# Optimization experiments

Hardware: AMD Instinct MI355X
Metric: run time of the kernel (lower is better)

## Reference

```python
import jax, jax.numpy as jnp
import numpy as np

N_NODES = 50000
N_EDGES = 800000
HID = 256
OUT = 128
NEG_SLOPE = 0.2


def gat_layer(x, src, dst, W_src, W_dst, a_src_vec, a_dst_vec, bias, n_nodes):
    # Dense projections (PyG lin_src / lin_dst for tuple in_channels)
    h_src = x @ W_src              # [N, C]
    h_dst = x @ W_dst              # [N, C]
    # Per-node attention logits (att_src/att_dst dot products)
    a_src = h_src @ a_src_vec      # [N]
    a_dst = h_dst @ a_dst_vec      # [N]
    # Edge logits + LeakyReLU
    e = jax.nn.leaky_relu(a_src[src] + a_dst[dst], NEG_SLOPE)  # [E]
    # Segment softmax over incoming edges of each dst node
    m = jax.ops.segment_max(e, dst, num_segments=n_nodes)      # [N]
    m = jnp.where(jnp.isfinite(m), m, 0.0)                      # empty segments
    ex = jnp.exp(e - m[dst])                                    # [E]
    s = jax.ops.segment_sum(ex, dst, num_segments=n_nodes)     # [N]
    alpha = ex / (s[dst] + 1e-16)                               # [E]
    # Attention-weighted message aggregation (scatter-add to dst)
    msg = alpha[:, None] * h_src[src]                           # [E, C]
    out = jax.ops.segment_sum(msg, dst, num_segments=n_nodes)  # [N, C]
    return out + bias


def setup_inputs() -> dict:
    key = jax.random.key(0)
    ks = jax.random.split(key, 12)
    x = jax.random.normal(ks[0], (N_NODES, HID), dtype=jnp.float32)
    edge_index = jax.random.randint(ks[1], (2, N_EDGES), 0, N_NODES, dtype=jnp.int64)
    sc1 = 1.0 / np.sqrt(HID)
    sc2 = 1.0 / np.sqrt(HID)
    return {
        "x": x,
        "edge_index": edge_index,
        "W1_src": jax.random.normal(ks[2], (HID, HID), dtype=jnp.float32) * sc1,
        "W1_dst": jax.random.normal(ks[3], (HID, HID), dtype=jnp.float32) * sc1,
        "att1_src": jax.random.normal(ks[4], (HID,), dtype=jnp.float32) * sc1,
        "att1_dst": jax.random.normal(ks[5], (HID,), dtype=jnp.float32) * sc1,
        "b1": jnp.zeros((HID,), dtype=jnp.float32),
        "W2_src": jax.random.normal(ks[6], (HID, OUT), dtype=jnp.float32) * sc2,
        "W2_dst": jax.random.normal(ks[7], (HID, OUT), dtype=jnp.float32) * sc2,
        "att2_src": jax.random.normal(ks[8], (OUT,), dtype=jnp.float32) * (1.0 / np.sqrt(OUT)),
        "att2_dst": jax.random.normal(ks[9], (OUT,), dtype=jnp.float32) * (1.0 / np.sqrt(OUT)),
        "b2": jnp.zeros((OUT,), dtype=jnp.float32),
    }


def reference(x, edge_index, W1_src, W1_dst, att1_src, att1_dst, b1,
              W2_src, W2_dst, att2_src, att2_dst, b2):
    src, dst = edge_index[0], edge_index[1]
    h = gat_layer(x, src, dst, W1_src, W1_dst, att1_src, att1_dst, b1, N_NODES)
    h = jax.nn.relu(h)
    out = gat_layer(h, src, dst, W2_src, W2_dst, att2_src, att2_dst, b2, N_NODES)
    return out
```

## Files before the change

### kernel.cpp

```cpp
#include <hip/hip_runtime.h>
#include <math.h>

#define N_NODES 50000
#define N_EDGES 800000
#define HID 256
#define OUT_C 128
#define NEG_SLOPE 0.2f
#define SCAN_NB ((N_NODES + 255) / 256)

typedef __attribute__((ext_vector_type(8))) short bf16x8;
typedef __attribute__((ext_vector_type(4))) float f32x4;
typedef _Float16 half_t;
typedef __attribute__((ext_vector_type(4))) _Float16 half4;
typedef __attribute__((ext_vector_type(2))) _Float16 half2t;

__device__ inline unsigned short bf16_rne(float x) {
    unsigned u = __float_as_uint(x);
    return (unsigned short)((u + 0x7fffu + ((u >> 16) & 1u)) >> 16);
}

__device__ __forceinline__ void async_copy16(const void* g, void* l) {
    __builtin_amdgcn_global_load_lds(
        (const __attribute__((address_space(1))) unsigned int*)g,
        (__attribute__((address_space(3))) unsigned int*)l, 16, 0, 0);
}


__global__ __launch_bounds__(256) void hist_rank_kernel(
    const int* __restrict__ dst, int* __restrict__ counts, int* __restrict__ rank) {
    int e = blockIdx.x * 256 + threadIdx.x;
    if (e < N_EDGES) rank[e] = atomicAdd(&counts[dst[e]], 1);
}

__global__ __launch_bounds__(256) void block_scan_kernel(
    const int* __restrict__ counts, int* __restrict__ excl,
    int* __restrict__ blockSums, int n) {
    __shared__ int waveSums[4];
    int i = blockIdx.x * 256 + threadIdx.x;
    int lane = threadIdx.x & 63;
    int wv = threadIdx.x >> 6;
    int c = (i < n) ? counts[i] : 0;
    int v = c;
    #pragma unroll
    for (int off = 1; off < 64; off <<= 1) {
        int t = __shfl_up(v, off);
        if (lane >= off) v += t;
    }
    if (lane == 63) waveSums[wv] = v;
    __syncthreads();
    int waveOff = 0;
    #pragma unroll
    for (int w = 0; w < 4; w++)
        if (w < wv) waveOff += waveSums[w];
    if (i < n) excl[i] = waveOff + v - c;
    if (threadIdx.x == 255) blockSums[blockIdx.x] = waveOff + v;
}

__global__ __launch_bounds__(256) void add_offsets_kernel(
    int* __restrict__ excl, const int* __restrict__ blockSums, int n) {
    __shared__ int lds[4];
    int tid = threadIdx.x;
    int partial = 0;
    for (int j = tid; j < (int)blockIdx.x; j += 256) partial += blockSums[j];
    #pragma unroll
    for (int off = 32; off > 0; off >>= 1) partial += __shfl_down(partial, off);
    if ((tid & 63) == 0) lds[tid >> 6] = partial;
    __syncthreads();
    int prefix = lds[0] + lds[1] + lds[2] + lds[3];
    int i = blockIdx.x * 256 + tid;
    if (i < n) excl[i] += prefix;
    if (i == 0) excl[n] = N_EDGES;
}

__global__ __launch_bounds__(256) void scatter_kernel(
    const int* __restrict__ src, const int* __restrict__ dst,
    const int* __restrict__ offsets, const int* __restrict__ rank,
    int* __restrict__ src_sorted) {
    int e = blockIdx.x * 256 + threadIdx.x;
    if (e >= N_EDGES) return;
    src_sorted[offsets[dst[e]] + rank[e]] = src[e];
}


__global__ __launch_bounds__(64) void compute_v_all_kernel(
    const float* __restrict__ W1s, const float* __restrict__ att1s,
    const float* __restrict__ W1d, const float* __restrict__ att1d,
    const float* __restrict__ W2s, const float* __restrict__ att2s,
    const float* __restrict__ W2d, const float* __restrict__ att2d,
    float* __restrict__ v1s, float* __restrict__ v1d,
    float* __restrict__ v2s, float* __restrict__ v2d) {
    int k = blockIdx.x;
    int lane = threadIdx.x;
    const float* W; const float* att; float* v; int cout;
    switch (blockIdx.y) {
        case 0: W = W1s; att = att1s; v = v1s; cout = HID; break;
        case 1: W = W1d; att = att1d; v = v1d; cout = HID; break;
        case 2: W = W2s; att = att2s; v = v2s; cout = OUT_C; break;
        default: W = W2d; att = att2d; v = v2d; cout = OUT_C; break;
    }
    float sum = 0.f;
    for (int j = lane; j < cout; j += 64)
        sum += W[k * cout + j] * att[j];
    #pragma unroll
    for (int off = 32; off > 0; off >>= 1)
        sum += __shfl_down(sum, off);
    if (lane == 0) v[k] = sum;
}


#define PACK1_T (8 * 17 * 64)
#define PACK2_T (8 * 9 * 64)

__global__ __launch_bounds__(256) void pack_all_kernel(
    const float* __restrict__ W1, const float* __restrict__ v1s, const float* __restrict__ v1d,
    const float* __restrict__ W2, const float* __restrict__ v2s, const float* __restrict__ v2d,
    unsigned short* __restrict__ hi1, unsigned short* __restrict__ lo1,
    unsigned short* __restrict__ hi2, unsigned short* __restrict__ lo2) {
    int t = blockIdx.x * 256 + threadIdx.x;
    const float *W, *vs, *vd; unsigned short *hi, *lo; int cout, NTL, tt;
    if (t < PACK1_T)            { tt = t;           W = W1; vs = v1s; vd = v1d; hi = hi1; lo = lo1; cout = HID;  NTL = 17; }
    else if (t < PACK1_T + PACK2_T) { tt = t - PACK1_T; W = W2; vs = v2s; vd = v2d; hi = hi2; lo = lo2; cout = OUT_C; NTL = 9; }
    else return;
    int lane = tt & 63;
    int tile = (tt >> 6) % NTL;
    int ks = tt / (64 * NTL);
    int m = lane & 15;
    int kbase = ks * 32 + (lane >> 4) * 8;
    #pragma unroll
    for (int j = 0; j < 8; j++) {
        float val;
        if (tile < NTL - 1) val = W[(kbase + j) * cout + tile * 16 + m];
        else val = (m == 0) ? vs[kbase + j] : (m == 1) ? vd[kbase + j] : 0.f;
        unsigned short h = bf16_rne(val);
        hi[tt * 8 + j] = h;
        lo[tt * 8 + j] = bf16_rne(val - __uint_as_float((unsigned)h << 16));
    }
}


template <int COUT, int NT, bool WRITE_A>
__device__ __forceinline__ void gemm_body(
    const float* __restrict__ A, const unsigned short* __restrict__ Bhi,
    const unsigned short* __restrict__ Blo, half_t* __restrict__ H,
    float* __restrict__ a_s, float* __restrict__ a_d, int M, int tile0,
    short* sBh, short* sBl) {
    const int NTL = COUT / 16 + 1;
    int wave = threadIdx.x >> 6, lane = threadIdx.x & 63;
    int m = lane & 15, quad = lane >> 4;
    int row0 = blockIdx.x * 128 + wave * 32;
    f32x4 acc[2][NT];
    #pragma unroll
    for (int rg = 0; rg < 2; rg++)
        #pragma unroll
        for (int nt = 0; nt < NT; nt++)
            acc[rg][nt] = (f32x4){0.f, 0.f, 0.f, 0.f};

    const float* arow[2];
    #pragma unroll
    for (int rg = 0; rg < 2; rg++) {
        int r = row0 + rg * 16 + m;
        if (r >= M) r = M - 1;
        arow[rg] = A + (size_t)r * HID;
    }

    for (int ks = 0; ks < 8; ks++) {
        __syncthreads();
        for (int u = wave; u < 2 * NT; u += 4) {
            int nt = (u < NT) ? u : u - NT;
            int tile = (WRITE_A && nt == NT - 1) ? (COUT / 16) : (tile0 + nt);
            size_t goff = ((size_t)(ks * NTL + tile) * 64 + lane) * 8;
            if (u < NT) async_copy16(Bhi + goff, sBh + nt * 512);
            else        async_copy16(Blo + goff, sBl + nt * 512);
        }
        __syncthreads();

        bf16x8 ah[2], al[2];
        #pragma unroll
        for (int rg = 0; rg < 2; rg++) {
            const float* ap = arow[rg] + ks * 32 + quad * 8;
            float4 v0 = *(const float4*)ap;
            float4 v1 = *(const float4*)(ap + 4);
            float av[8] = {v0.x, v0.y, v0.z, v0.w, v1.x, v1.y, v1.z, v1.w};
            #pragma unroll
            for (int j = 0; j < 8; j++) {
                unsigned short h = bf16_rne(av[j]);
                float hf = __uint_as_float((unsigned)h << 16);
                ah[rg][j] = (short)h;
                al[rg][j] = (short)bf16_rne(av[j] - hf);
            }
        }
        #pragma unroll
        for (int nt = 0; nt < NT; nt++) {
            bf16x8 bh = *(const bf16x8*)(sBh + nt * 512 + lane * 8);
            bf16x8 bl = *(const bf16x8*)(sBl + nt * 512 + lane * 8);
            acc[0][nt] = __builtin_amdgcn_mfma_f32_16x16x32_bf16(ah[0], bh, acc[0][nt], 0, 0, 0);
            acc[1][nt] = __builtin_amdgcn_mfma_f32_16x16x32_bf16(ah[1], bh, acc[1][nt], 0, 0, 0);
            acc[0][nt] = __builtin_amdgcn_mfma_f32_16x16x32_bf16(ah[0], bl, acc[0][nt], 0, 0, 0);
            acc[1][nt] = __builtin_amdgcn_mfma_f32_16x16x32_bf16(ah[1], bl, acc[1][nt], 0, 0, 0);
            acc[0][nt] = __builtin_amdgcn_mfma_f32_16x16x32_bf16(al[0], bh, acc[0][nt], 0, 0, 0);
            acc[1][nt] = __builtin_amdgcn_mfma_f32_16x16x32_bf16(al[1], bh, acc[1][nt], 0, 0, 0);
        }
    }
    const int NW = WRITE_A ? NT - 1 : NT;
    #pragma unroll
    for (int rg = 0; rg < 2; rg++)
        #pragma unroll
        for (int nt = 0; nt < NW; nt++)
            #pragma unroll
            for (int r = 0; r < 4; r++) {
                int row = row0 + rg * 16 + quad * 4 + r;
                if (row < M)
                    H[(size_t)row * COUT + (tile0 + nt) * 16 + m] = (half_t)acc[rg][nt][r];
            }
    if (WRITE_A) {
        #pragma unroll
        for (int rg = 0; rg < 2; rg++)
            #pragma unroll
            for (int r = 0; r < 4; r++) {
                int row = row0 + rg * 16 + quad * 4 + r;
                if (row < M) {
                    if (m == 0) a_s[row] = acc[rg][NT - 1][r];
                    else if (m == 1) a_d[row] = acc[rg][NT - 1][r];
                }
            }
    }
}

template <int COUT>
__global__ __launch_bounds__(256) void mfma_gemm_a_kernel(
    const float* __restrict__ A, const unsigned short* __restrict__ Bhi,
    const unsigned short* __restrict__ Blo, half_t* __restrict__ H,
    float* __restrict__ a_s, float* __restrict__ a_d, int M) {
    __shared__ short sBh[9 * 512];
    __shared__ short sBl[9 * 512];
    if (blockIdx.y == 0)
        gemm_body<COUT, 9, true>(A, Bhi, Blo, H, a_s, a_d, M, 0, sBh, sBl);
    else
        gemm_body<COUT, 8, false>(A, Bhi, Blo, H, a_s, a_d, M, 8, sBh, sBl);
}


template <int C, bool RELU>
__global__ __launch_bounds__(256) void fused_aggregate_kernel(
    const int* __restrict__ offsets, const int* __restrict__ src_sorted,
    const float* __restrict__ a_src, const float* __restrict__ a_dst,
    const half_t* __restrict__ h, const float* __restrict__ bias,
    float* __restrict__ out) {
    constexpr int CH = 8;
    int node = (int)((blockIdx.x * 256u + threadIdx.x) >> 6);
    int lane = threadIdx.x & 63;
    if (node >= N_NODES) return;
    int beg = offsets[node], end = offsets[node + 1];
    float ad = a_dst[node];
    float s = 0.f;

    if (C == 256) {
        float4 acc = make_float4(0.f, 0.f, 0.f, 0.f);
        for (int base = beg; base < end; base += CH) {
            int cnt = end - base; if (cnt > CH) cnt = CH;
            int idx[CH];
            #pragma unroll
            for (int j = 0; j < CH; j++)
                idx[j] = src_sorted[(j < cnt) ? base + j : base];
            half4 hv[CH];
            #pragma unroll
            for (int j = 0; j < CH; j++)
                hv[j] = *(const half4*)(h + ((unsigned)idx[j] * C + lane * 4));
            float w[CH];
            #pragma unroll
            for (int j = 0; j < CH; j++) {
                float l = a_src[idx[j]] + ad;
                l = fmaxf(l, l * NEG_SLOPE);
                w[j] = (j < cnt) ? __expf(l) : 0.f;
                s += w[j];
            }
            #pragma unroll
            for (int j = 0; j < CH; j++) {
                acc.x += w[j] * (float)hv[j][0]; acc.y += w[j] * (float)hv[j][1];
                acc.z += w[j] * (float)hv[j][2]; acc.w += w[j] * (float)hv[j][3];
            }
        }
        float inv = 1.f / (s + 1e-16f);
        float4 bv = *(const float4*)(bias + lane * 4);
        acc.x = acc.x * inv + bv.x; acc.y = acc.y * inv + bv.y;
        acc.z = acc.z * inv + bv.z; acc.w = acc.w * inv + bv.w;
        if (RELU) {
            acc.x = fmaxf(acc.x, 0.f); acc.y = fmaxf(acc.y, 0.f);
            acc.z = fmaxf(acc.z, 0.f); acc.w = fmaxf(acc.w, 0.f);
        }
        *(float4*)(out + (size_t)node * C + lane * 4) = acc;
    } else {
        float2 acc = make_float2(0.f, 0.f);
        for (int base = beg; base < end; base += CH) {
            int cnt = end - base; if (cnt > CH) cnt = CH;
            int idx[CH];
            #pragma unroll
            for (int j = 0; j < CH; j++)
                idx[j] = src_sorted[(j < cnt) ? base + j : base];
            half2t hv[CH];
            #pragma unroll
            for (int j = 0; j < CH; j++)
                hv[j] = *(const half2t*)(h + ((unsigned)idx[j] * C + lane * 2));
            float w[CH];
            #pragma unroll
            for (int j = 0; j < CH; j++) {
                float l = a_src[idx[j]] + ad;
                l = fmaxf(l, l * NEG_SLOPE);
                w[j] = (j < cnt) ? __expf(l) : 0.f;
                s += w[j];
            }
            #pragma unroll
            for (int j = 0; j < CH; j++) {
                acc.x += w[j] * (float)hv[j][0]; acc.y += w[j] * (float)hv[j][1];
            }
        }
        float inv = 1.f / (s + 1e-16f);
        float2 bv = *(const float2*)(bias + lane * 2);
        acc.x = acc.x * inv + bv.x; acc.y = acc.y * inv + bv.y;
        if (RELU) { acc.x = fmaxf(acc.x, 0.f); acc.y = fmaxf(acc.y, 0.f); }
        *(float2*)(out + (size_t)node * C + lane * 2) = acc;
    }
}

extern "C" void kernel_launch(void* const* d_in, const int* in_sizes, int n_in,
                              void* d_out, int out_size, void* d_ws, size_t ws_size,
                              hipStream_t stream) {
    const float* x     = (const float*)d_in[0];
    const int*   edge  = (const int*)d_in[1];
    const int*   src   = edge;
    const int*   dst   = edge + N_EDGES;
    const float* W1s   = (const float*)d_in[2];
    const float* W1d   = (const float*)d_in[3];
    const float* att1s = (const float*)d_in[4];
    const float* att1d = (const float*)d_in[5];
    const float* b1    = (const float*)d_in[6];
    const float* W2s   = (const float*)d_in[7];
    const float* W2d   = (const float*)d_in[8];
    const float* att2s = (const float*)d_in[9];
    const float* att2d = (const float*)d_in[10];
    const float* b2    = (const float*)d_in[11];
    float* out = (float*)d_out;

    float* ws    = (float*)d_ws;
    half_t* h1   = (half_t*)ws;
    float* act2  = ws + (size_t)N_NODES * HID;
    float* a_s   = act2 + (size_t)N_NODES * HID;
    float* a_d   = a_s + N_NODES;
    float* vbuf  = a_d + N_NODES;
    int* ibase      = (int*)(vbuf + 4 * HID);
    int* src_sorted = ibase;
    int* rank       = src_sorted + N_EDGES;
    int* counts     = rank + N_EDGES;
    int* offsets    = counts + N_NODES;
    int* blockSums  = offsets + N_NODES + 1;
    unsigned short* wp1h = (unsigned short*)(((uintptr_t)(blockSums + SCAN_NB) + 15) & ~(uintptr_t)15);
    unsigned short* wp1l = wp1h + PACK1_T * 8;
    unsigned short* wp2h = wp1l + PACK1_T * 8;
    unsigned short* wp2l = wp2h + PACK2_T * 8;
    float* v1s = vbuf, *v1d = vbuf + HID, *v2s = vbuf + 2 * HID, *v2d = vbuf + 3 * HID;
    half_t* h2 = h1;

    const int edgeBlocks = (N_EDGES + 255) / 256;
    const int waveBlocksN = (N_NODES + 3) / 4;
    const int gemmBlocks = (N_NODES + 127) / 128;

    hipMemsetAsync(counts, 0, N_NODES * sizeof(int), stream);
    hist_rank_kernel<<<edgeBlocks, 256, 0, stream>>>(dst, counts, rank);
    block_scan_kernel<<<SCAN_NB, 256, 0, stream>>>(counts, offsets, blockSums, N_NODES);
    add_offsets_kernel<<<SCAN_NB, 256, 0, stream>>>(offsets, blockSums, N_NODES);
    scatter_kernel<<<edgeBlocks, 256, 0, stream>>>(src, dst, offsets, rank, src_sorted);

    compute_v_all_kernel<<<dim3(HID, 4), 64, 0, stream>>>(
        W1s, att1s, W1d, att1d, W2s, att2s, W2d, att2d, v1s, v1d, v2s, v2d);
    pack_all_kernel<<<(PACK1_T + PACK2_T + 255) / 256, 256, 0, stream>>>(
        W1s, v1s, v1d, W2s, v2s, v2d, wp1h, wp1l, wp2h, wp2l);

    mfma_gemm_a_kernel<HID><<<dim3(gemmBlocks, 2), 256, 0, stream>>>(
        x, wp1h, wp1l, h1, a_s, a_d, N_NODES);
    fused_aggregate_kernel<HID, true><<<waveBlocksN, 256, 0, stream>>>(
        offsets, src_sorted, a_s, a_d, h1, b1, act2);

    mfma_gemm_a_kernel<OUT_C><<<dim3(gemmBlocks, 1), 256, 0, stream>>>(
        act2, wp2h, wp2l, h2, a_s, a_d, N_NODES);
    fused_aggregate_kernel<OUT_C, false><<<waveBlocksN, 256, 0, stream>>>(
        offsets, src_sorted, a_s, a_d, h2, b2, out);
}
```

Baseline: 323.7 us.

## Fuse prep kernels, compute all GEMM tiles per block, double-buffer B tiles

Merges the edge scatter, attention-vector projection and weight packing into one prep kernel, folding the W·att dot products directly into packing. The layer GEMM now computes every output tile in a single block instead of splitting columns across grid.y, so each block loads and splits its A rows only once. B tiles are double-buffered in LDS so the next k-step's async copy overlaps the current MFMAs. This raises per-block accumulator registers and LDS use, and halves the block count for the first layer, which may reduce occupancy.

```diff
diff --git a/kernel.cpp b/kernel.cpp
--- a/kernel.cpp
+++ b/kernel.cpp
@@ -72,55 +72,37 @@
     if (i == 0) excl[n] = N_EDGES;
 }
 
-__global__ __launch_bounds__(256) void scatter_kernel(
+
+#define PACK1_T (8 * 17 * 64)
+#define PACK2_T (8 * 9 * 64)
+#define EDGE_BLOCKS ((N_EDGES + 255) / 256)
+#define PACK_BLOCKS ((PACK1_T + PACK2_T + 255) / 256)
+
+__global__ __launch_bounds__(256) void prep_kernel(
     const int* __restrict__ src, const int* __restrict__ dst,
     const int* __restrict__ offsets, const int* __restrict__ rank,
-    int* __restrict__ src_sorted) {
-    int e = blockIdx.x * 256 + threadIdx.x;
-    if (e >= N_EDGES) return;
-    src_sorted[offsets[dst[e]] + rank[e]] = src[e];
-}
-
-
-__global__ __launch_bounds__(64) void compute_v_all_kernel(
+    int* __restrict__ src_sorted,
     const float* __restrict__ W1s, const float* __restrict__ att1s,
     const float* __restrict__ W1d, const float* __restrict__ att1d,
     const float* __restrict__ W2s, const float* __restrict__ att2s,
     const float* __restrict__ W2d, const float* __restrict__ att2d,
-    float* __restrict__ v1s, float* __restrict__ v1d,
-    float* __restrict__ v2s, float* __restrict__ v2d) {
-    int k = blockIdx.x;
-    int lane = threadIdx.x;
-    const float* W; const float* att; float* v; int cout;
-    switch (blockIdx.y) {
-        case 0: W = W1s; att = att1s; v = v1s; cout = HID; break;
-        case 1: W = W1d; att = att1d; v = v1d; cout = HID; break;
-        case 2: W = W2s; att = att2s; v = v2s; cout = OUT_C; break;
-        default: W = W2d; att = att2d; v = v2d; cout = OUT_C; break;
-    }
-    float sum = 0.f;
-    for (int j = lane; j < cout; j += 64)
-        sum += W[k * cout + j] * att[j];
-    #pragma unroll
-    for (int off = 32; off > 0; off >>= 1)
-        sum += __shfl_down(sum, off);
-    if (lane == 0) v[k] = sum;
-}
-
-
-#define PACK1_T (8 * 17 * 64)
-#define PACK2_T (8 * 9 * 64)
-
-__global__ __launch_bounds__(256) void pack_all_kernel(
-    const float* __restrict__ W1, const float* __restrict__ v1s, const float* __restrict__ v1d,
-    const float* __restrict__ W2, const float* __restrict__ v2s, const float* __restrict__ v2d,
     unsigned short* __restrict__ hi1, unsigned short* __restrict__ lo1,
     unsigned short* __restrict__ hi2, unsigned short* __restrict__ lo2) {
-    int t = blockIdx.x * 256 + threadIdx.x;
-    const float *W, *vs, *vd; unsigned short *hi, *lo; int cout, NTL, tt;
-    if (t < PACK1_T)            { tt = t;           W = W1; vs = v1s; vd = v1d; hi = hi1; lo = lo1; cout = HID;  NTL = 17; }
-    else if (t < PACK1_T + PACK2_T) { tt = t - PACK1_T; W = W2; vs = v2s; vd = v2d; hi = hi2; lo = lo2; cout = OUT_C; NTL = 9; }
-    else return;
+    if (blockIdx.x < EDGE_BLOCKS) {
+        int e = blockIdx.x * 256 + threadIdx.x;
+        if (e < N_EDGES)
+            src_sorted[offsets[dst[e]] + rank[e]] = src[e];
+        return;
+    }
+    int t = (blockIdx.x - EDGE_BLOCKS) * 256 + threadIdx.x;
+    const float *W, *Ws, *Wd, *avs, *avd; unsigned short *hi, *lo; int cout, NTL, tt;
+    if (t < PACK1_T) {
+        tt = t; W = W1s; Ws = W1s; Wd = W1d; avs = att1s; avd = att1d;
+        hi = hi1; lo = lo1; cout = HID; NTL = 17;
+    } else if (t < PACK1_T + PACK2_T) {
+        tt = t - PACK1_T; W = W2s; Ws = W2s; Wd = W2d; avs = att2s; avd = att2d;
+        hi = hi2; lo = lo2; cout = OUT_C; NTL = 9;
+    } else return;
     int lane = tt & 63;
     int tile = (tt >> 6) % NTL;
     int ks = tt / (64 * NTL);
@@ -129,8 +111,19 @@
     #pragma unroll
     for (int j = 0; j < 8; j++) {
         float val;
-        if (tile < NTL - 1) val = W[(kbase + j) * cout + tile * 16 + m];
-        else val = (m == 0) ? vs[kbase + j] : (m == 1) ? vd[kbase + j] : 0.f;
+        if (tile < NTL - 1) {
+            val = W[(size_t)(kbase + j) * cout + tile * 16 + m];
+        } else if (m < 2) {
+            const float* Wr = ((m == 0) ? Ws : Wd) + (size_t)(kbase + j) * cout;
+            const float* av = (m == 0) ? avs : avd;
+            float s = 0.f;
+            for (int jj = 0; jj < cout; jj += 4) {
+                float4 w4 = *(const float4*)(Wr + jj);
+                float4 a4 = *(const float4*)(av + jj);
+                s += w4.x * a4.x + w4.y * a4.y + w4.z * a4.z + w4.w * a4.w;
+            }
+            val = s;
+        } else val = 0.f;
         unsigned short h = bf16_rne(val);
         hi[tt * 8 + j] = h;
         lo[tt * 8 + j] = bf16_rne(val - __uint_as_float((unsigned)h << 16));
@@ -138,13 +131,14 @@
 }
 
 
-template <int COUT, int NT, bool WRITE_A>
-__device__ __forceinline__ void gemm_body(
+template <int COUT>
+__global__ __launch_bounds__(256) void mfma_gemm_kernel(
     const float* __restrict__ A, const unsigned short* __restrict__ Bhi,
     const unsigned short* __restrict__ Blo, half_t* __restrict__ H,
-    float* __restrict__ a_s, float* __restrict__ a_d, int M, int tile0,
-    short* sBh, short* sBl) {
-    const int NTL = COUT / 16 + 1;
+    float* __restrict__ a_s, float* __restrict__ a_d, int M) {
+    constexpr int NT = COUT / 16 + 1;
+    __shared__ short sBh[2 * NT * 512];
+    __shared__ short sBl[2 * NT * 512];
     int wave = threadIdx.x >> 6, lane = threadIdx.x & 63;
     int m = lane & 15, quad = lane >> 4;
     int row0 = blockIdx.x * 128 + wave * 32;
@@ -163,16 +157,20 @@
         arow[rg] = A + (size_t)r * HID;
     }
 
-    for (int ks = 0; ks < 8; ks++) {
-        __syncthreads();
+    auto STAGE = [&](int ks, int b) {
         for (int u = wave; u < 2 * NT; u += 4) {
             int nt = (u < NT) ? u : u - NT;
-            int tile = (WRITE_A && nt == NT - 1) ? (COUT / 16) : (tile0 + nt);
-            size_t goff = ((size_t)(ks * NTL + tile) * 64 + lane) * 8;
-            if (u < NT) async_copy16(Bhi + goff, sBh + nt * 512);
-            else        async_copy16(Blo + goff, sBl + nt * 512);
-        }
-        __syncthreads();
+            size_t goff = ((size_t)(ks * NT + nt) * 64 + lane) * 8;
+            if (u < NT) async_copy16(Bhi + goff, sBh + b * NT * 512 + nt * 512);
+            else        async_copy16(Blo + goff, sBl + b * NT * 512 + nt * 512);
+        }
+    };
+
+    STAGE(0, 0);
+    __syncthreads();
+    int cur = 0;
+    for (int ks = 0; ks < 8; ks++) {
+        if (ks < 7) STAGE(ks + 1, cur ^ 1);
 
         bf16x8 ah[2], al[2];
         #pragma unroll
@@ -191,8 +189,8 @@
         }
         #pragma unroll
         for (int nt = 0; nt < NT; nt++) {
-            bf16x8 bh = *(const bf16x8*)(sBh + nt * 512 + lane * 8);
-            bf16x8 bl = *(const bf16x8*)(sBl + nt * 512 + lane * 8);
+            bf16x8 bh = *(const bf16x8*)(sBh + cur * NT * 512 + nt * 512 + lane * 8);
+            bf16x8 bl = *(const bf16x8*)(sBl + cur * NT * 512 + nt * 512 + lane * 8);
             acc[0][nt] = __builtin_amdgcn_mfma_f32_16x16x32_bf16(ah[0], bh, acc[0][nt], 0, 0, 0);
             acc[1][nt] = __builtin_amdgcn_mfma_f32_16x16x32_bf16(ah[1], bh, acc[1][nt], 0, 0, 0);
             acc[0][nt] = __builtin_amdgcn_mfma_f32_16x16x32_bf16(ah[0], bl, acc[0][nt], 0, 0, 0);
@@ -200,43 +198,29 @@
             acc[0][nt] = __builtin_amdgcn_mfma_f32_16x16x32_bf16(al[0], bh, acc[0][nt], 0, 0, 0);
             acc[1][nt] = __builtin_amdgcn_mfma_f32_16x16x32_bf16(al[1], bh, acc[1][nt], 0, 0, 0);
         }
-    }
-    const int NW = WRITE_A ? NT - 1 : NT;
+        __syncthreads();
+        cur ^= 1;
+    }
     #pragma unroll
     for (int rg = 0; rg < 2; rg++)
         #pragma unroll
-        for (int nt = 0; nt < NW; nt++)
+        for (int nt = 0; nt < NT - 1; nt++)
             #pragma unroll
             for (int r = 0; r < 4; r++) {
                 int row = row0 + rg * 16 + quad * 4 + r;
                 if (row < M)
-                    H[(size_t)row * COUT + (tile0 + nt) * 16 + m] = (half_t)acc[rg][nt][r];
-            }
-    if (WRITE_A) {
-        #pragma unroll
-        for (int rg = 0; rg < 2; rg++)
-            #pragma unroll
-            for (int r = 0; r < 4; r++) {
-                int row = row0 + rg * 16 + quad * 4 + r;
-                if (row < M) {
-                    if (m == 0) a_s[row] = acc[rg][NT - 1][r];
-                    else if (m == 1) a_d[row] = acc[rg][NT - 1][r];
-                }
-            }
-    }
-}
-
-template <int COUT>
-__global__ __launch_bounds__(256) void mfma_gemm_a_kernel(
-    const float* __restrict__ A, const unsigned short* __restrict__ Bhi,
-    const unsigned short* __restrict__ Blo, half_t* __restrict__ H,
-    float* __restrict__ a_s, float* __restrict__ a_d, int M) {
-    __shared__ short sBh[9 * 512];
-    __shared__ short sBl[9 * 512];
-    if (blockIdx.y == 0)
-        gemm_body<COUT, 9, true>(A, Bhi, Blo, H, a_s, a_d, M, 0, sBh, sBl);
-    else
-        gemm_body<COUT, 8, false>(A, Bhi, Blo, H, a_s, a_d, M, 8, sBh, sBl);
+                    H[(size_t)row * COUT + nt * 16 + m] = (half_t)acc[rg][nt][r];
+            }
+    #pragma unroll
+    for (int rg = 0; rg < 2; rg++)
+        #pragma unroll
+        for (int r = 0; r < 4; r++) {
+            int row = row0 + rg * 16 + quad * 4 + r;
+            if (row < M) {
+                if (m == 0) a_s[row] = acc[rg][NT - 1][r];
+                else if (m == 1) a_d[row] = acc[rg][NT - 1][r];
+            }
+        }
 }
 
 
@@ -346,8 +330,7 @@
     float* act2  = ws + (size_t)N_NODES * HID;
     float* a_s   = act2 + (size_t)N_NODES * HID;
     float* a_d   = a_s + N_NODES;
-    float* vbuf  = a_d + N_NODES;
-    int* ibase      = (int*)(vbuf + 4 * HID);
+    int* ibase      = (int*)(a_d + N_NODES);
     int* src_sorted = ibase;
     int* rank       = src_sorted + N_EDGES;
     int* counts     = rank + N_EDGES;
@@ -357,30 +340,27 @@
     unsigned short* wp1l = wp1h + PACK1_T * 8;
     unsigned short* wp2h = wp1l + PACK1_T * 8;
     unsigned short* wp2l = wp2h + PACK2_T * 8;
-    float* v1s = vbuf, *v1d = vbuf + HID, *v2s = vbuf + 2 * HID, *v2d = vbuf + 3 * HID;
     half_t* h2 = h1;
 
-    const int edgeBlocks = (N_EDGES + 255) / 256;
     const int waveBlocksN = (N_NODES + 3) / 4;
     const int gemmBlocks = (N_NODES + 127) / 128;
 
     hipMemsetAsync(counts, 0, N_NODES * sizeof(int), stream);
-    hist_rank_kernel<<<edgeBlocks, 256, 0, stream>>>(dst, counts, rank);
+    hist_rank_kernel<<<EDGE_BLOCKS, 256, 0, stream>>>(dst, counts, rank);
     block_scan_kernel<<<SCAN_NB, 256, 0, stream>>>(counts, offsets, blockSums, N_NODES);
     add_offsets_kernel<<<SCAN_NB, 256, 0, stream>>>(offsets, blockSums, N_NODES);
-    scatter_kernel<<<edgeBlocks, 256, 0, stream>>>(src, dst, offsets, rank, src_sorted);
-
-    compute_v_all_kernel<<<dim3(HID, 4), 64, 0, stream>>>(
-        W1s, att1s, W1d, att1d, W2s, att2s, W2d, att2d, v1s, v1d, v2s, v2d);
-    pack_all_kernel<<<(PACK1_T + PACK2_T + 255) / 256, 256, 0, stream>>>(
-        W1s, v1s, v1d, W2s, v2s, v2d, wp1h, wp1l, wp2h, wp2l);
-
-    mfma_gemm_a_kernel<HID><<<dim3(gemmBlocks, 2), 256, 0, stream>>>(
+
+    prep_kernel<<<EDGE_BLOCKS + PACK_BLOCKS, 256, 0, stream>>>(
+        src, dst, offsets, rank, src_sorted,
+        W1s, att1s, W1d, att1d, W2s, att2s, W2d, att2d,
+        wp1h, wp1l, wp2h, wp2l);
+
+    mfma_gemm_kernel<HID><<<gemmBlocks, 256, 0, stream>>>(
         x, wp1h, wp1l, h1, a_s, a_d, N_NODES);
     fused_aggregate_kernel<HID, true><<<waveBlocksN, 256, 0, stream>>>(
         offsets, src_sorted, a_s, a_d, h1, b1, act2);
 
-    mfma_gemm_a_kernel<OUT_C><<<dim3(gemmBlocks, 1), 256, 0, stream>>>(
+    mfma_gemm_kernel<OUT_C><<<gemmBlocks, 256, 0, stream>>>(
         act2, wp2h, wp2l, h2, a_s, a_d, N_NODES);
     fused_aggregate_kernel<OUT_C, false><<<waveBlocksN, 256, 0, stream>>>(
         offsets, src_sorted, a_s, a_d, h2, b2, out);
```

Result: slower. 390.6 us (+20.7%).

## Double-buffer LDS weight tiles and compute all GEMM output tiles per block

Applied to the files above, without the earlier changes.

The projection GEMM now keeps two LDS buffers for the packed bf16 hi/lo weight tiles, so the async copies for the next k-step overlap the MFMA work on the current one. This replaces the two barriers per k-step with one. It also drops the two-way column split for the 256-wide layer: each block computes all 17 output tiles, including the attention-logit tile, so every A row is loaded and split into bf16 hi/lo only once. The cost is roughly double the accumulator registers and LDS per block for layer 1, which can lower occupancy, and half as many blocks in that launch.

```diff
diff --git a/kernel.cpp b/kernel.cpp
--- a/kernel.cpp
+++ b/kernel.cpp
@@ -138,13 +138,14 @@
 }
 
 
-template <int COUT, int NT, bool WRITE_A>
-__device__ __forceinline__ void gemm_body(
+template <int COUT>
+__global__ __launch_bounds__(256) void mfma_gemm_kernel(
     const float* __restrict__ A, const unsigned short* __restrict__ Bhi,
     const unsigned short* __restrict__ Blo, half_t* __restrict__ H,
-    float* __restrict__ a_s, float* __restrict__ a_d, int M, int tile0,
-    short* sBh, short* sBl) {
-    const int NTL = COUT / 16 + 1;
+    float* __restrict__ a_s, float* __restrict__ a_d, int M) {
+    constexpr int NT = COUT / 16 + 1;
+    __shared__ short sBh[2 * NT * 512];
+    __shared__ short sBl[2 * NT * 512];
     int wave = threadIdx.x >> 6, lane = threadIdx.x & 63;
     int m = lane & 15, quad = lane >> 4;
     int row0 = blockIdx.x * 128 + wave * 32;
@@ -163,16 +164,20 @@
         arow[rg] = A + (size_t)r * HID;
     }
 
-    for (int ks = 0; ks < 8; ks++) {
-        __syncthreads();
+    auto STAGE = [&](int ks, int b) {
         for (int u = wave; u < 2 * NT; u += 4) {
             int nt = (u < NT) ? u : u - NT;
-            int tile = (WRITE_A && nt == NT - 1) ? (COUT / 16) : (tile0 + nt);
-            size_t goff = ((size_t)(ks * NTL + tile) * 64 + lane) * 8;
-            if (u < NT) async_copy16(Bhi + goff, sBh + nt * 512);
-            else        async_copy16(Blo + goff, sBl + nt * 512);
-        }
-        __syncthreads();
+            size_t goff = ((size_t)(ks * NT + nt) * 64 + lane) * 8;
+            if (u < NT) async_copy16(Bhi + goff, sBh + b * NT * 512 + nt * 512);
+            else        async_copy16(Blo + goff, sBl + b * NT * 512 + nt * 512);
+        }
+    };
+
+    STAGE(0, 0);
+    __syncthreads();
+    int cur = 0;
+    for (int ks = 0; ks < 8; ks++) {
+        if (ks < 7) STAGE(ks + 1, cur ^ 1);
 
         bf16x8 ah[2], al[2];
         #pragma unroll
@@ -191,8 +196,8 @@
         }
         #pragma unroll
         for (int nt = 0; nt < NT; nt++) {
-            bf16x8 bh = *(const bf16x8*)(sBh + nt * 512 + lane * 8);
-            bf16x8 bl = *(const bf16x8*)(sBl + nt * 512 + lane * 8);
+            bf16x8 bh = *(const bf16x8*)(sBh + cur * NT * 512 + nt * 512 + lane * 8);
+            bf16x8 bl = *(const bf16x8*)(sBl + cur * NT * 512 + nt * 512 + lane * 8);
             acc[0][nt] = __builtin_amdgcn_mfma_f32_16x16x32_bf16(ah[0], bh, acc[0][nt], 0, 0, 0);
             acc[1][nt] = __builtin_amdgcn_mfma_f32_16x16x32_bf16(ah[1], bh, acc[1][nt], 0, 0, 0);
             acc[0][nt] = __builtin_amdgcn_mfma_f32_16x16x32_bf16(ah[0], bl, acc[0][nt], 0, 0, 0);
@@ -200,43 +205,29 @@
             acc[0][nt] = __builtin_amdgcn_mfma_f32_16x16x32_bf16(al[0], bh, acc[0][nt], 0, 0, 0);
             acc[1][nt] = __builtin_amdgcn_mfma_f32_16x16x32_bf16(al[1], bh, acc[1][nt], 0, 0, 0);
         }
-    }
-    const int NW = WRITE_A ? NT - 1 : NT;
+        __syncthreads();
+        cur ^= 1;
+    }
     #pragma unroll
     for (int rg = 0; rg < 2; rg++)
         #pragma unroll
-        for (int nt = 0; nt < NW; nt++)
+        for (int nt = 0; nt < NT - 1; nt++)
             #pragma unroll
             for (int r = 0; r < 4; r++) {
                 int row = row0 + rg * 16 + quad * 4 + r;
                 if (row < M)
-                    H[(size_t)row * COUT + (tile0 + nt) * 16 + m] = (half_t)acc[rg][nt][r];
-            }
-    if (WRITE_A) {
-        #pragma unroll
-        for (int rg = 0; rg < 2; rg++)
-            #pragma unroll
-            for (int r = 0; r < 4; r++) {
-                int row = row0 + rg * 16 + quad * 4 + r;
-                if (row < M) {
-                    if (m == 0) a_s[row] = acc[rg][NT - 1][r];
-                    else if (m == 1) a_d[row] = acc[rg][NT - 1][r];
-                }
-            }
-    }
-}
-
-template <int COUT>
-__global__ __launch_bounds__(256) void mfma_gemm_a_kernel(
-    const float* __restrict__ A, const unsigned short* __restrict__ Bhi,
-    const unsigned short* __restrict__ Blo, half_t* __restrict__ H,
-    float* __restrict__ a_s, float* __restrict__ a_d, int M) {
-    __shared__ short sBh[9 * 512];
-    __shared__ short sBl[9 * 512];
-    if (blockIdx.y == 0)
-        gemm_body<COUT, 9, true>(A, Bhi, Blo, H, a_s, a_d, M, 0, sBh, sBl);
-    else
-        gemm_body<COUT, 8, false>(A, Bhi, Blo, H, a_s, a_d, M, 8, sBh, sBl);
+                    H[(size_t)row * COUT + nt * 16 + m] = (half_t)acc[rg][nt][r];
+            }
+    #pragma unroll
+    for (int rg = 0; rg < 2; rg++)
+        #pragma unroll
+        for (int r = 0; r < 4; r++) {
+            int row = row0 + rg * 16 + quad * 4 + r;
+            if (row < M) {
+                if (m == 0) a_s[row] = acc[rg][NT - 1][r];
+                else if (m == 1) a_d[row] = acc[rg][NT - 1][r];
+            }
+        }
 }
 
 
@@ -375,12 +366,12 @@
     pack_all_kernel<<<(PACK1_T + PACK2_T + 255) / 256, 256, 0, stream>>>(
         W1s, v1s, v1d, W2s, v2s, v2d, wp1h, wp1l, wp2h, wp2l);
 
-    mfma_gemm_a_kernel<HID><<<dim3(gemmBlocks, 2), 256, 0, stream>>>(
+    mfma_gemm_kernel<HID><<<gemmBlocks, 256, 0, stream>>>(
         x, wp1h, wp1l, h1, a_s, a_d, N_NODES);
     fused_aggregate_kernel<HID, true><<<waveBlocksN, 256, 0, stream>>>(
         offsets, src_sorted, a_s, a_d, h1, b1, act2);
 
-    mfma_gemm_a_kernel<OUT_C><<<dim3(gemmBlocks, 1), 256, 0, stream>>>(
+    mfma_gemm_kernel<OUT_C><<<gemmBlocks, 256, 0, stream>>>(
         act2, wp2h, wp2l, h2, a_s, a_d, N_NODES);
     fused_aggregate_kernel<OUT_C, false><<<waveBlocksN, 256, 0, stream>>>(
         offsets, src_sorted, a_s, a_d, h2, b2, out);
```

After: 340.9 us. 5.3% more time.
